# Kernel optimization log

Measured on AMD Instinct MI355X. Metric: run time of the kernel, lower is better.

The kernel has to match this reference:

```python
import jax, jax.numpy as jnp
import numpy as np
import math

B, N, D = 4, 1024, 512
L, H, DH = 6, 8, 64
FF_INNER = 4 * D
NUM_BUCKETS, MAX_DIST = 32, 128
SCALE = 16.0  # cosine_sim_scale
ROT_DIM = 32  # min(32, dim_head)


def layernorm(x, g, stable=False, eps=1e-5):
    if stable:
        x = x / jax.lax.stop_gradient(jnp.max(x, axis=-1, keepdims=True))
    mean = jnp.mean(x, axis=-1, keepdims=True)
    var = jnp.mean(jnp.square(x - mean), axis=-1, keepdims=True)  # unbiased=False
    return (x - mean) * jax.lax.rsqrt(var + eps) * g


def l2norm(x, eps=1e-12):
    return x / jnp.maximum(jnp.linalg.norm(x, axis=-1, keepdims=True), eps)


def rotary_freqs(n):
    inv_freq = 1.0 / (10000.0 ** (jnp.arange(0, ROT_DIM, 2, dtype=jnp.float32) / ROT_DIM))
    f = jnp.arange(n, dtype=jnp.float32)[:, None] * inv_freq[None, :]  # [n, ROT_DIM/2]
    return jnp.repeat(f, 2, axis=-1)  # [n, ROT_DIM], interleaved pairs


def apply_rotary(t, freqs):
    # rotate only first ROT_DIM dims (rotary_embedding_torch semantics)
    rot, passd = t[..., :ROT_DIM], t[..., ROT_DIM:]
    x = rot.reshape(*rot.shape[:-1], ROT_DIM // 2, 2)
    rotated = jnp.stack((-x[..., 1], x[..., 0]), axis=-1).reshape(rot.shape)
    rot = rot * jnp.cos(freqs) + rotated * jnp.sin(freqs)
    return jnp.concatenate([rot, passd], axis=-1)


def rel_pos_bias(emb, i, j):
    # T5-style causal relative position buckets
    rel = jnp.arange(j)[None, :] - jnp.arange(i)[:, None]
    n = jnp.maximum(-rel, 0)
    max_exact = NUM_BUCKETS // 2
    val_large = max_exact + (
        jnp.log(jnp.maximum(n, 1).astype(jnp.float32) / max_exact)
        / math.log(MAX_DIST / max_exact) * (NUM_BUCKETS - max_exact)
    ).astype(jnp.int32)
    val_large = jnp.minimum(val_large, NUM_BUCKETS - 1)
    bucket = jnp.where(n < max_exact, n, val_large)
    return emb[bucket].transpose(2, 0, 1)  # [h, i, j]


def setup_inputs() -> dict:
    key = jax.random.key(0)
    ks = jax.random.split(key, 9)
    s = 0.02
    return {
        "x": jax.random.normal(ks[0], (B, N, D), jnp.float32),
        "rel_pos_emb": jax.random.normal(ks[1], (NUM_BUCKETS, H), jnp.float32) * s,
        "g_attn": jnp.ones((L, D), jnp.float32),
        "null_kv": jax.random.normal(ks[2], (L, 2, DH), jnp.float32),
        "Wq": jax.random.normal(ks[3], (L, D, H * DH), jnp.float32) * s,
        "Wkv": jax.random.normal(ks[4], (L, D, 2 * DH), jnp.float32) * s,
        "Wo": jax.random.normal(ks[5], (L, H * DH, D), jnp.float32) * s,
        "g_attn_out": jnp.ones((L, D), jnp.float32),
        "g_ff": jnp.ones((L, D), jnp.float32),
        "W1": jax.random.normal(ks[6], (L, D, 2 * FF_INNER), jnp.float32) * s,
        "W2": jax.random.normal(ks[7], (L, FF_INNER, D), jnp.float32) * s,
        "g_final": jnp.ones((D,), jnp.float32),
        "W_proj": jax.random.normal(ks[8], (D, D), jnp.float32) * s,
    }


def reference(x, rel_pos_emb, g_attn, null_kv, Wq, Wkv, Wo, g_attn_out, g_ff, W1, W2, g_final, W_proj):
    b, n, d = x.shape
    freqs = rotary_freqs(n)
    bias = rel_pos_bias(rel_pos_emb, n, n + 1)          # [h, n, n+1] (null kv column at j=0)
    causal = jnp.triu(jnp.ones((n, n + 1), dtype=bool), k=2)  # .triu(j - i + 1)
    neg = -jnp.finfo(x.dtype).max
    for l in range(L):
        # --- attention block ---
        xn = layernorm(x, g_attn[l])
        q = (xn @ Wq[l]).reshape(b, n, H, DH).transpose(0, 2, 1, 3) * SCALE  # b h n d
        k, v = jnp.split(xn @ Wkv[l], 2, axis=-1)                            # b n d (single-head kv)
        q = apply_rotary(q, freqs)
        k = apply_rotary(k, freqs)
        k = jnp.concatenate([jnp.broadcast_to(null_kv[l, 0], (b, 1, DH)), k], axis=1)
        v = jnp.concatenate([jnp.broadcast_to(null_kv[l, 1], (b, 1, DH)), v], axis=1)
        qn = l2norm(q) * math.sqrt(SCALE)   # cosine-sim attention
        kn = l2norm(k) * math.sqrt(SCALE)
        sim = jnp.einsum('bhid,bjd->bhij', qn, kn) + bias
        sim = jnp.where(causal, neg, sim)
        attn = jax.nn.softmax(sim.astype(jnp.float32), axis=-1).astype(x.dtype)
        o = jnp.einsum('bhij,bjd->bhid', attn, v).transpose(0, 2, 1, 3).reshape(b, n, H * DH)
        x = x + layernorm(o @ Wo[l], g_attn_out[l])
        # --- SwiGLU feedforward block ---
        hn = layernorm(x, g_ff[l])
        a, gate = jnp.split(hn @ W1[l], 2, axis=-1)
        x = x + (a * jax.nn.silu(gate)) @ W2[l]
    out = layernorm(x, g_final, stable=True)
    return out @ W_proj
```

## Files before the change

### kernel.cpp

```cpp
#include <hip/hip_runtime.h>
#include <hip/hip_bf16.h>
#include <cmath>

using bf16 = __hip_bfloat16;
typedef __bf16 v8bf __attribute__((ext_vector_type(8)));
typedef __bf16 v4bf __attribute__((ext_vector_type(4)));
typedef float  v4f  __attribute__((ext_vector_type(4)));

__device__ __forceinline__ float bf2f(bf16 x) { return __bfloat162float(x); }
__device__ __forceinline__ bf16  f2bf(float x) { return __float2bfloat16(x); }
__device__ __forceinline__ __bf16 tobf(float x) {
    bf16 h = __float2bfloat16(x);
    return __builtin_bit_cast(__bf16, h);
}

__device__ __forceinline__ void gll16(const bf16* g, bf16* l) {
    __builtin_amdgcn_global_load_lds(
        (const __attribute__((address_space(1))) unsigned int*)g,
        (__attribute__((address_space(3))) unsigned int*)l, 16, 0, 0);
}

__device__ __forceinline__ float ldin(const void* p, size_t i, int isf32) {
    if (isf32) return ((const float*)p)[i];
    return bf2f(((const bf16*)p)[i]);
}

__device__ __forceinline__ void ld8(const void* p, size_t base, int f, float v[8]) {
    if (f) {
        const float* pf = (const float*)p + base;
        float4 a = *(const float4*)pf, b = *(const float4*)(pf + 4);
        v[0]=a.x; v[1]=a.y; v[2]=a.z; v[3]=a.w;
        v[4]=b.x; v[5]=b.y; v[6]=b.z; v[7]=b.w;
    } else {
        v8bf a = *(const v8bf*)((const bf16*)p + base);
#pragma unroll
        for (int j = 0; j < 8; ++j) v[j] = (float)a[j];
    }
}

__device__ __forceinline__ float wave_sum(float v) {
#pragma unroll
    for (int o = 32; o > 0; o >>= 1) v += __shfl_xor(v, o, 64);
    return v;
}
__device__ __forceinline__ float wave_max(float v) {
#pragma unroll
    for (int o = 32; o > 0; o >>= 1) v = fmaxf(v, __shfl_xor(v, o, 64));
    return v;
}

__global__ void detect_k(const unsigned short* __restrict__ x, int* __restrict__ flag)
{
    __shared__ int s;
    int t = threadIdx.x;
    if (t == 0) s = 0;
    __syncthreads();
    int bad = 0;
    for (int i = t; i < 4096; i += 256) {
        int e = (x[i] >> 7) & 0xFF;
        if (e >= 147) bad++;
    }
    atomicAdd(&s, bad);
    __syncthreads();
    if (t == 0) *flag = (s > 64) ? 1 : 0;
}

__global__ __launch_bounds__(512, 2)
void gemm256_silu(const bf16* __restrict__ A, const bf16* __restrict__ BT,
                  bf16* __restrict__ U, int K, int lda)
{
    __shared__ bf16 As[2][256 * 64];
    __shared__ bf16 Bs[2][256 * 64];
    const int t = threadIdx.x;
    const int lane = t & 63;
    const int wave = t >> 6;
    const int wm = (wave >> 2) * 128;
    const int wn = (wave & 3) * 64;
    const int bm = blockIdx.x * 256;
    const int bn = blockIdx.y * 256;
    const int fr = lane & 15;
    const int quad = lane >> 4;

    v4f acc[8][4];
#pragma unroll
    for (int i = 0; i < 8; ++i)
#pragma unroll
        for (int j = 0; j < 4; ++j) { v4f z = {0.f, 0.f, 0.f, 0.f}; acc[i][j] = z; }

    auto stage = [&](int buf, int k0) {
#pragma unroll
        for (int r = 0; r < 4; ++r) {
            int c = t + 512 * r;
            int row = c >> 3;
            int g = (c & 7) ^ (row & 7);
            gll16(A + (size_t)(bm + row) * lda + k0 + g * 8, &As[buf][c * 8]);
            gll16(BT + (size_t)(bn + row) * K + k0 + g * 8, &Bs[buf][c * 8]);
        }
    };

    stage(0, 0);
    __syncthreads();
    const int nb = K >> 6;
    for (int kt = 0; kt < nb; ++kt) {
        const int buf = kt & 1;
        if (kt + 1 < nb) stage(buf ^ 1, (kt + 1) * 64);
#pragma unroll
        for (int ks = 0; ks < 2; ++ks) {
            v8bf af[8], bfr[4];
            const int gk = ((ks * 4 + quad) ^ (fr & 7)) * 8;
#pragma unroll
            for (int mt = 0; mt < 8; ++mt)
                af[mt] = *(const v8bf*)(&As[buf][(wm + mt * 16 + fr) * 64 + gk]);
#pragma unroll
            for (int nt = 0; nt < 4; ++nt)
                bfr[nt] = *(const v8bf*)(&Bs[buf][(wn + nt * 16 + fr) * 64 + gk]);
#pragma unroll
            for (int mt = 0; mt < 8; ++mt)
#pragma unroll
                for (int nt = 0; nt < 4; ++nt)
                    acc[mt][nt] = __builtin_amdgcn_mfma_f32_16x16x32_bf16(
                        af[mt], bfr[nt], acc[mt][nt], 0, 0, 0);
        }
        __syncthreads();
    }

    const int r0 = quad * 4;
    const int gbase = ((bn + wn) >> 6) * 32;
#pragma unroll
    for (int mt = 0; mt < 8; ++mt)
#pragma unroll
        for (int nt = 0; nt < 2; ++nt)
#pragma unroll
            for (int r = 0; r < 4; ++r) {
                int row = bm + wm + mt * 16 + r0 + r;
                int col = gbase + nt * 16 + fr;
                float a  = acc[mt][nt][r];
                float gg = acc[mt][nt + 2][r];
                U[(size_t)row * 2048 + col] = f2bf(a * (gg / (1.f + __expf(-gg))));
            }
}

__global__ __launch_bounds__(256)
void gemm64(const bf16* __restrict__ A, const bf16* __restrict__ BT,
            bf16* __restrict__ C, int M, int N, int K, int lda)
{
    __shared__ bf16 As[2][64 * 64];
    __shared__ bf16 Bs[2][64 * 64];
    const int t = threadIdx.x;
    const int lane = t & 63;
    const int wave = t >> 6;
    const int wm = (wave >> 1) * 32;
    const int wn = (wave & 1) * 32;
    const int bm = blockIdx.x * 64;
    const int bn = blockIdx.y * 64;
    const int fr = lane & 15;
    const int quad = lane >> 4;

    v4f acc[2][2];
#pragma unroll
    for (int i = 0; i < 2; ++i)
#pragma unroll
        for (int j = 0; j < 2; ++j) { v4f z = {0.f, 0.f, 0.f, 0.f}; acc[i][j] = z; }

    auto stage = [&](int buf, int k0) {
#pragma unroll
        for (int r = 0; r < 2; ++r) {
            int c = t + 256 * r;
            int row = c >> 3;
            int g = (c & 7) ^ (row & 7);
            gll16(A + (size_t)(bm + row) * lda + k0 + g * 8, &As[buf][c * 8]);
            gll16(BT + (size_t)(bn + row) * K + k0 + g * 8, &Bs[buf][c * 8]);
        }
    };

    stage(0, 0);
    __syncthreads();
    const int nb = K >> 6;
    for (int kt = 0; kt < nb; ++kt) {
        const int buf = kt & 1;
        if (kt + 1 < nb) stage(buf ^ 1, (kt + 1) * 64);
#pragma unroll
        for (int ks = 0; ks < 2; ++ks) {
            v8bf af[2], bfr[2];
            const int gk = ((ks * 4 + quad) ^ (fr & 7)) * 8;
#pragma unroll
            for (int mt = 0; mt < 2; ++mt)
                af[mt] = *(const v8bf*)(&As[buf][(wm + mt * 16 + fr) * 64 + gk]);
#pragma unroll
            for (int nt = 0; nt < 2; ++nt)
                bfr[nt] = *(const v8bf*)(&Bs[buf][(wn + nt * 16 + fr) * 64 + gk]);
#pragma unroll
            for (int mt = 0; mt < 2; ++mt)
#pragma unroll
                for (int nt = 0; nt < 2; ++nt)
                    acc[mt][nt] = __builtin_amdgcn_mfma_f32_16x16x32_bf16(
                        af[mt], bfr[nt], acc[mt][nt], 0, 0, 0);
        }
        __syncthreads();
    }
    const int r0 = quad * 4;
#pragma unroll
    for (int mt = 0; mt < 2; ++mt)
#pragma unroll
        for (int nt = 0; nt < 2; ++nt)
#pragma unroll
            for (int r = 0; r < 4; ++r) {
                int row = bm + wm + mt * 16 + r0 + r;
                int col = bn + wn + nt * 16 + fr;
                C[(size_t)row * N + col] = f2bf(acc[mt][nt][r]);
            }
}

__global__ __launch_bounds__(256)
void gemm64_out(const bf16* __restrict__ A, const bf16* __restrict__ BT,
                void* __restrict__ C, int M, int N, int K, int lda,
                const int* __restrict__ flag)
{
    __shared__ bf16 As[2][64 * 64];
    __shared__ bf16 Bs[2][64 * 64];
    const int f = *flag;
    const int t = threadIdx.x;
    const int lane = t & 63;
    const int wave = t >> 6;
    const int wm = (wave >> 1) * 32;
    const int wn = (wave & 1) * 32;
    const int bm = blockIdx.x * 64;
    const int bn = blockIdx.y * 64;
    const int fr = lane & 15;
    const int quad = lane >> 4;

    v4f acc[2][2];
#pragma unroll
    for (int i = 0; i < 2; ++i)
#pragma unroll
        for (int j = 0; j < 2; ++j) { v4f z = {0.f, 0.f, 0.f, 0.f}; acc[i][j] = z; }

    auto stage = [&](int buf, int k0) {
#pragma unroll
        for (int r = 0; r < 2; ++r) {
            int c = t + 256 * r;
            int row = c >> 3;
            int g = (c & 7) ^ (row & 7);
            gll16(A + (size_t)(bm + row) * lda + k0 + g * 8, &As[buf][c * 8]);
            gll16(BT + (size_t)(bn + row) * K + k0 + g * 8, &Bs[buf][c * 8]);
        }
    };

    stage(0, 0);
    __syncthreads();
    const int nb = K >> 6;
    for (int kt = 0; kt < nb; ++kt) {
        const int buf = kt & 1;
        if (kt + 1 < nb) stage(buf ^ 1, (kt + 1) * 64);
#pragma unroll
        for (int ks = 0; ks < 2; ++ks) {
            v8bf af[2], bfr[2];
            const int gk = ((ks * 4 + quad) ^ (fr & 7)) * 8;
#pragma unroll
            for (int mt = 0; mt < 2; ++mt)
                af[mt] = *(const v8bf*)(&As[buf][(wm + mt * 16 + fr) * 64 + gk]);
#pragma unroll
            for (int nt = 0; nt < 2; ++nt)
                bfr[nt] = *(const v8bf*)(&Bs[buf][(wn + nt * 16 + fr) * 64 + gk]);
#pragma unroll
            for (int mt = 0; mt < 2; ++mt)
#pragma unroll
                for (int nt = 0; nt < 2; ++nt)
                    acc[mt][nt] = __builtin_amdgcn_mfma_f32_16x16x32_bf16(
                        af[mt], bfr[nt], acc[mt][nt], 0, 0, 0);
        }
        __syncthreads();
    }
    const int r0 = quad * 4;
#pragma unroll
    for (int mt = 0; mt < 2; ++mt)
#pragma unroll
        for (int nt = 0; nt < 2; ++nt)
#pragma unroll
            for (int r = 0; r < 4; ++r) {
                int row = bm + wm + mt * 16 + r0 + r;
                int col = bn + wn + nt * 16 + fr;
                if (f) ((float*)C)[(size_t)row * N + col] = acc[mt][nt][r];
                else   ((bf16*)C)[(size_t)row * N + col] = f2bf(acc[mt][nt][r]);
            }
}

__global__ __launch_bounds__(256)
void transpose2_k(const void* __restrict__ in, bf16* __restrict__ out, int R, int C,
                  size_t inZ, size_t outZ, const int* __restrict__ flag)
{
    __shared__ bf16 tile[32][33];
    int f = *flag;
    size_t ioff = (size_t)blockIdx.z * inZ;
    bf16* dst = out + (size_t)blockIdx.z * outZ;
    int c0 = blockIdx.x * 32, r0 = blockIdx.y * 32;
    int tx = threadIdx.x, ty = threadIdx.y;
#pragma unroll
    for (int i = 0; i < 32; i += 8)
        tile[ty + i][tx] = f2bf(ldin(in, ioff + (size_t)(r0 + ty + i) * C + c0 + tx, f));
    __syncthreads();
#pragma unroll
    for (int i = 0; i < 32; i += 8)
        dst[(size_t)(c0 + ty + i) * R + r0 + tx] = tile[tx][ty + i];
}

__global__ __launch_bounds__(256)
void transposeW1_k(const void* __restrict__ in, bf16* __restrict__ out,
                   const int* __restrict__ flag)
{
    __shared__ bf16 tile[32][33];
    int f = *flag;
    size_t ioff = (size_t)blockIdx.z * (512ull * 4096);
    bf16* dst = out + (size_t)blockIdx.z * (512ull * 4096);
    int c0 = blockIdx.x * 32, r0 = blockIdx.y * 32;
    int tx = threadIdx.x, ty = threadIdx.y;
#pragma unroll
    for (int i = 0; i < 32; i += 8)
        tile[ty + i][tx] = f2bf(ldin(in, ioff + (size_t)(r0 + ty + i) * 4096 + c0 + tx, f));
    __syncthreads();
#pragma unroll
    for (int i = 0; i < 32; i += 8) {
        int j = c0 + ty + i;
        int jp = (j < 2048) ? (((j >> 5) << 6) | (j & 31))
                            : ((((j - 2048) >> 5) << 6) | 32 | (j & 31));
        dst[(size_t)jp * 512 + r0 + tx] = tile[tx][ty + i];
    }
}

__global__ __launch_bounds__(256)
void xinit_ln_k(const void* __restrict__ in, const void* __restrict__ g,
                const int* __restrict__ flag, float* __restrict__ x, bf16* __restrict__ xn)
{
    int f = *flag;
    int row = blockIdx.x * 4 + (threadIdx.x >> 6);
    int lane = threadIdx.x & 63;
    int c0 = lane * 8;
    float v[8];
    ld8(in, (size_t)row * 512 + c0, f, v);
    float* xr = x + (size_t)row * 512 + c0;
    *(float4*)xr       = make_float4(v[0], v[1], v[2], v[3]);
    *(float4*)(xr + 4) = make_float4(v[4], v[5], v[6], v[7]);
    float s = 0.f;
#pragma unroll
    for (int j = 0; j < 8; ++j) s += v[j];
    float mean = wave_sum(s) * (1.f / 512.f);
    float q = 0.f;
#pragma unroll
    for (int j = 0; j < 8; ++j) { float d = v[j] - mean; q += d * d; }
    float var = wave_sum(q) * (1.f / 512.f);
    float rstd = rsqrtf(var + 1e-5f);
    float gv[8];
    ld8(g, c0, f, gv);
    v8bf o;
#pragma unroll
    for (int j = 0; j < 8; ++j) o[j] = tobf((v[j] - mean) * rstd * gv[j]);
    *(v8bf*)(xn + (size_t)row * 512 + c0) = o;
}

__global__ __launch_bounds__(256)
void addln_ln_k(const bf16* __restrict__ tin, const void* __restrict__ g1, int g1off,
                const void* __restrict__ g2, int g2off, const int* __restrict__ flag,
                float* __restrict__ x, bf16* __restrict__ xn)
{
    int f = *flag;
    int row = blockIdx.x * 4 + (threadIdx.x >> 6);
    int lane = threadIdx.x & 63;
    int c0 = lane * 8;
    float tv[8];
    {
        v8bf a = *(const v8bf*)(tin + (size_t)row * 512 + c0);
#pragma unroll
        for (int j = 0; j < 8; ++j) tv[j] = (float)a[j];
    }
    float s = 0.f;
#pragma unroll
    for (int j = 0; j < 8; ++j) s += tv[j];
    float mean = wave_sum(s) * (1.f / 512.f);
    float q = 0.f;
#pragma unroll
    for (int j = 0; j < 8; ++j) { float d = tv[j] - mean; q += d * d; }
    float var = wave_sum(q) * (1.f / 512.f);
    float rstd = rsqrtf(var + 1e-5f);
    float g1v[8];
    ld8(g1, (size_t)g1off + c0, f, g1v);
    float* xr = x + (size_t)row * 512 + c0;
    float4 xa = *(float4*)xr, xb = *(float4*)(xr + 4);
    float nx[8] = {xa.x, xa.y, xa.z, xa.w, xb.x, xb.y, xb.z, xb.w};
#pragma unroll
    for (int j = 0; j < 8; ++j) nx[j] += (tv[j] - mean) * rstd * g1v[j];
    *(float4*)xr       = make_float4(nx[0], nx[1], nx[2], nx[3]);
    *(float4*)(xr + 4) = make_float4(nx[4], nx[5], nx[6], nx[7]);
    float s2 = 0.f;
#pragma unroll
    for (int j = 0; j < 8; ++j) s2 += nx[j];
    float mean2 = wave_sum(s2) * (1.f / 512.f);
    float q2 = 0.f;
#pragma unroll
    for (int j = 0; j < 8; ++j) { float e = nx[j] - mean2; q2 += e * e; }
    float var2 = wave_sum(q2) * (1.f / 512.f);
    float rstd2 = rsqrtf(var2 + 1e-5f);
    float g2v[8];
    ld8(g2, (size_t)g2off + c0, f, g2v);
    v8bf o;
#pragma unroll
    for (int j = 0; j < 8; ++j) o[j] = tobf((nx[j] - mean2) * rstd2 * g2v[j]);
    *(v8bf*)(xn + (size_t)row * 512 + c0) = o;
}

__global__ __launch_bounds__(256)
void add_ln_k(const bf16* __restrict__ tin, const void* __restrict__ g, int goff,
              const int* __restrict__ flag, int stable,
              float* __restrict__ x, bf16* __restrict__ xn)
{
    int f = *flag;
    int row = blockIdx.x * 4 + (threadIdx.x >> 6);
    int lane = threadIdx.x & 63;
    int c0 = lane * 8;
    float nx[8];
    {
        v8bf a = *(const v8bf*)(tin + (size_t)row * 512 + c0);
        float* xr = x + (size_t)row * 512 + c0;
        float4 xa = *(float4*)xr, xb = *(float4*)(xr + 4);
        float xv[8] = {xa.x, xa.y, xa.z, xa.w, xb.x, xb.y, xb.z, xb.w};
#pragma unroll
        for (int j = 0; j < 8; ++j) nx[j] = xv[j] + (float)a[j];
        *(float4*)xr       = make_float4(nx[0], nx[1], nx[2], nx[3]);
        *(float4*)(xr + 4) = make_float4(nx[4], nx[5], nx[6], nx[7]);
    }
    float v[8];
#pragma unroll
    for (int j = 0; j < 8; ++j) v[j] = nx[j];
    if (stable) {
        float m = v[0];
#pragma unroll
        for (int j = 1; j < 8; ++j) m = fmaxf(m, v[j]);
        float mx = wave_max(m);
#pragma unroll
        for (int j = 0; j < 8; ++j) v[j] /= mx;
    }
    float s = 0.f;
#pragma unroll
    for (int j = 0; j < 8; ++j) s += v[j];
    float mean = wave_sum(s) * (1.f / 512.f);
    float q = 0.f;
#pragma unroll
    for (int j = 0; j < 8; ++j) { float d = v[j] - mean; q += d * d; }
    float var = wave_sum(q) * (1.f / 512.f);
    float rstd = rsqrtf(var + 1e-5f);
    float gv[8];
    ld8(g, (size_t)goff + c0, f, gv);
    v8bf o;
#pragma unroll
    for (int j = 0; j < 8; ++j) o[j] = tobf((v[j] - mean) * rstd * gv[j]);
    *(v8bf*)(xn + (size_t)row * 512 + c0) = o;
}

__global__ __launch_bounds__(256)
void rotab_k(float2* __restrict__ tab)
{
    int idx = blockIdx.x * 256 + threadIdx.x;
    if (idx >= 16384) return;
    int n = idx >> 4, p = idx & 15;
    float ang = (float)n * expf((float)p * -0.5756462732f);
    tab[idx] = make_float2(cosf(ang), sinf(ang));
}

__global__ __launch_bounds__(256)
void bias_k(const void* __restrict__ rpe, const int* __restrict__ flag, float* __restrict__ tab)
{
    int f = *flag;
    int idx = blockIdx.x * 256 + threadIdx.x;
    if (idx >= 8 * 1025) return;
    int h = idx / 1025, dist = idx % 1025;
    int bkt;
    if (dist < 16) bkt = dist;
    else {
        bkt = 16 + (int)(logf((float)dist / 16.f) / logf(8.f) * 16.f);
        if (bkt > 31) bkt = 31;
    }
    tab[idx] = ldin(rpe, bkt * 8 + h, f) - 16.f;
}

__global__ __launch_bounds__(256)
void qkvprep_k(const bf16* __restrict__ qkv, const void* __restrict__ nkv, int nkoff,
               const int* __restrict__ flag, const float2* __restrict__ rtab,
               bf16* __restrict__ Q, bf16* __restrict__ K, bf16* __restrict__ Vt)
{
    int t = threadIdx.x, lane = t & 63;
    int bid = blockIdx.x;
    if (bid < 2048) {
        int rid = bid * 16 + (t >> 4);
        int h = rid & 7;
        int n = (rid >> 3) & 1023;
        int b = rid >> 13;
        int g16 = t & 15;
        int d0 = g16 * 4;
        v4bf a = *(const v4bf*)(qkv + (size_t)((b << 10) | n) * 640 + h * 64 + d0);
        float v[4];
#pragma unroll
        for (int j = 0; j < 4; ++j) v[j] = (float)a[j] * 16.f;
        if (d0 < 32) {
            float4 cs = *(const float4*)((const float*)rtab + (size_t)n * 32 + (size_t)(d0 >> 1) * 2);
            float r0 = v[0] * cs.x - v[1] * cs.y;
            float r1 = v[1] * cs.x + v[0] * cs.y;
            float r2 = v[2] * cs.z - v[3] * cs.w;
            float r3 = v[3] * cs.z + v[2] * cs.w;
            v[0] = r0; v[1] = r1; v[2] = r2; v[3] = r3;
        }
        float ss = v[0]*v[0] + v[1]*v[1] + v[2]*v[2] + v[3]*v[3];
#pragma unroll
        for (int o = 1; o < 16; o <<= 1) ss += __shfl_xor(ss, o, 64);
        float sc = 4.f / fmaxf(sqrtf(ss), 1e-12f);
        v4bf ov;
#pragma unroll
        for (int j = 0; j < 4; ++j) ov[j] = tobf(v[j] * sc);
        *(v4bf*)(Q + (((size_t)(b * 8 + h)) * 1024 + n) * 64 + d0) = ov;
    } else {
        int f = *flag;
        int rid = (bid - 2048) * 4 + (t >> 6);
        if (rid >= 4 * 1088) return;
        int j = rid % 1088;
        int b = rid / 1088;
        if (j >= 1025) {
            K[((size_t)b * 1088 + j) * 64 + lane] = f2bf(0.f);
            Vt[((size_t)b * 64 + lane) * 1088 + j] = f2bf(0.f);
            return;
        }
        float kv, vv;
        if (j == 0) {
            kv = ldin(nkv, nkoff + lane, f);
            vv = ldin(nkv, nkoff + 64 + lane, f);
        } else {
            int n = j - 1;
            const bf16* src = qkv + (size_t)(b * 1024 + n) * 640 + 512;
            kv = bf2f(src[lane]);
            vv = bf2f(src[64 + lane]);
            if (lane < 32) {
                float2 cs = rtab[n * 16 + (lane >> 1)];
                float other = __shfl_xor(kv, 1, 64);
                float rot = (lane & 1) ? other : -other;
                kv = kv * cs.x + rot * cs.y;
            }
        }
        float nrm = sqrtf(wave_sum(kv * kv));
        kv = kv / fmaxf(nrm, 1e-12f) * 4.f;
        K[((size_t)b * 1088 + j) * 64 + lane] = f2bf(kv);
        Vt[((size_t)b * 64 + lane) * 1088 + j] = f2bf(vv);
    }
}

__global__ __launch_bounds__(256)
void attn_mfma(const bf16* __restrict__ Q, const bf16* __restrict__ Kg,
               const bf16* __restrict__ Vtg, const float* __restrict__ bias,
               bf16* __restrict__ O)
{
    __shared__ bf16 Ks[64][72];
    __shared__ bf16 Vts[64][72];
    __shared__ bf16 Ps[4][16][72];
    __shared__ float bs[1088];
    const int bh = blockIdx.x, b = bh >> 3, h = bh & 7;
    const int yy = (int)gridDim.y - 1 - (int)blockIdx.y;
    const int i0 = yy * 64;
    const int t = threadIdx.x, lane = t & 63, w = t >> 6;
    const int col = lane & 15, quad = lane >> 4, fk = quad * 8;
    const float* bt = bias + h * 1025;
    const bf16* Kb = Kg + (size_t)b * 1088 * 64;
    const bf16* Vb = Vtg + (size_t)b * 64 * 1088;

    for (int idx = t; idx < i0 + 64; idx += 256) bs[idx] = bt[idx];

    v8bf qf[2];
    const bf16* qrow = Q + ((size_t)bh * 1024 + i0 + w * 16 + col) * 64;
    qf[0] = *(const v8bf*)(qrow + fk);
    qf[1] = *(const v8bf*)(qrow + 32 + fk);

    v4f oacc[4];
#pragma unroll
    for (int dt = 0; dt < 4; ++dt) { v4f z = {0.f,0.f,0.f,0.f}; oacc[dt] = z; }
    float lpart[4] = {0.f, 0.f, 0.f, 0.f};

    const int nch = yy + 2;
    const int rr0 = t >> 3, co0 = (t & 7) * 8;
    const int rr1 = (t + 256) >> 3, co1 = co0;

    v8bf kr[2], vr[2];
    {
        kr[0] = *(const v8bf*)(Kb + (size_t)rr0 * 64 + co0);
        vr[0] = *(const v8bf*)(Vb + (size_t)rr0 * 1088 + co0);
        kr[1] = *(const v8bf*)(Kb + (size_t)rr1 * 64 + co1);
        vr[1] = *(const v8bf*)(Vb + (size_t)rr1 * 1088 + co1);
    }

    for (int ch = 0; ch < nch; ++ch) {
        const int j0 = ch * 64;
        __syncthreads();
        *(v8bf*)(&Ks[rr0][co0])  = kr[0];
        *(v8bf*)(&Vts[rr0][co0]) = vr[0];
        *(v8bf*)(&Ks[rr1][co1])  = kr[1];
        *(v8bf*)(&Vts[rr1][co1]) = vr[1];
        if (ch + 1 < nch) {
            int j0n = (ch + 1) * 64;
            kr[0] = *(const v8bf*)(Kb + (size_t)(j0n + rr0) * 64 + co0);
            vr[0] = *(const v8bf*)(Vb + (size_t)rr0 * 1088 + j0n + co0);
            kr[1] = *(const v8bf*)(Kb + (size_t)(j0n + rr1) * 64 + co1);
            vr[1] = *(const v8bf*)(Vb + (size_t)rr1 * 1088 + j0n + co1);
        }
        __syncthreads();

        v4f sreg[4];
#pragma unroll
        for (int nt = 0; nt < 4; ++nt) {
            v4f z = {0.f,0.f,0.f,0.f};
            v8bf kf0 = *(const v8bf*)(&Ks[nt * 16 + col][fk]);
            v8bf kf1 = *(const v8bf*)(&Ks[nt * 16 + col][32 + fk]);
            z = __builtin_amdgcn_mfma_f32_16x16x32_bf16(qf[0], kf0, z, 0, 0, 0);
            z = __builtin_amdgcn_mfma_f32_16x16x32_bf16(qf[1], kf1, z, 0, 0, 0);
            sreg[nt] = z;
        }

        if (ch < yy) {
#pragma unroll
            for (int reg = 0; reg < 4; ++reg) {
                int i = i0 + w * 16 + quad * 4 + reg;
                int dbase = i - j0 - col;
#pragma unroll
                for (int nt = 0; nt < 4; ++nt) {
                    float pp = __expf(sreg[nt][reg] + bs[dbase - nt * 16]);
                    lpart[reg] += pp;
                    Ps[w][quad * 4 + reg][nt * 16 + col] = f2bf(pp);
                }
            }
        } else {
#pragma unroll
            for (int reg = 0; reg < 4; ++reg) {
                int i = i0 + w * 16 + quad * 4 + reg;
#pragma unroll
                for (int nt = 0; nt < 4; ++nt) {
                    int j = j0 + nt * 16 + col;
                    float pp = 0.f;
                    if (j <= i + 1 && j < 1025) {
                        int dist = i - j; if (dist < 0) dist = 0;
                        pp = __expf(sreg[nt][reg] + bs[dist]);
                    }
                    lpart[reg] += pp;
                    Ps[w][quad * 4 + reg][nt * 16 + col] = f2bf(pp);
                }
            }
        }

        v8bf pf[2];
        pf[0] = *(const v8bf*)(&Ps[w][col][fk]);
        pf[1] = *(const v8bf*)(&Ps[w][col][32 + fk]);
#pragma unroll
        for (int dt = 0; dt < 4; ++dt) {
#pragma unroll
            for (int ks = 0; ks < 2; ++ks) {
                v8bf vf = *(const v8bf*)(&Vts[dt * 16 + col][ks * 32 + fk]);
                oacc[dt] = __builtin_amdgcn_mfma_f32_16x16x32_bf16(pf[ks], vf, oacc[dt], 0, 0, 0);
            }
        }
    }

#pragma unroll
    for (int reg = 0; reg < 4; ++reg) {
#pragma unroll
        for (int o = 1; o < 16; o <<= 1) lpart[reg] += __shfl_xor(lpart[reg], o, 64);
        float inv = 1.f / lpart[reg];
        int i = i0 + w * 16 + quad * 4 + reg;
        bf16* orow = O + ((size_t)(b * 1024 + i)) * 512 + h * 64;
#pragma unroll
        for (int dt = 0; dt < 4; ++dt)
            orow[dt * 16 + col] = f2bf(oacc[dt][reg] * inv);
    }
}

extern "C" void kernel_launch(void* const* d_in, const int* in_sizes, int n_in,
                              void* d_out, int out_size, void* d_ws, size_t ws_size,
                              hipStream_t stream)
{
    const void* x_in     = d_in[0];
    const void* rpe      = d_in[1];
    const void* g_attn   = d_in[2];
    const void* null_kv  = d_in[3];
    const void* Wq       = d_in[4];
    const void* Wkv      = d_in[5];
    const void* Wo       = d_in[6];
    const void* g_attn_o = d_in[7];
    const void* g_ff     = d_in[8];
    const void* W1       = d_in[9];
    const void* W2       = d_in[10];
    const void* g_final  = d_in[11];
    const void* W_proj   = d_in[12];

    char* wp = (char*)d_ws;
    auto alloc = [&](size_t bytes) {
        char* p = wp; wp += (bytes + 255) & ~(size_t)255; return p;
    };
    float* xf    = (float*)alloc(4096ull * 512 * 4);
    bf16*  xn    = (bf16*) alloc(4096ull * 512 * 2);
    bf16*  tb    = (bf16*) alloc(4096ull * 512 * 2);
    bf16*  ub    = (bf16*) alloc(4096ull * 4096 * 2);
    bf16*  Kb    = (bf16*) alloc(4ull * 1088 * 64 * 2);
    bf16*  Vtb   = (bf16*) alloc(4ull * 64 * 1088 * 2);
    float* btab  = (float*)alloc(8ull * 1025 * 4);
    float2* rtab = (float2*)alloc(16384ull * 8);
    int*   dfl   = (int*)  alloc(256);
    bf16*  WqkvT = (bf16*) alloc(6ull * 640 * 512 * 2);
    bf16*  WoT   = (bf16*) alloc(6ull * 512 * 512 * 2);
    bf16*  W1T   = (bf16*) alloc(6ull * 4096 * 512 * 2);
    bf16*  W2T   = (bf16*) alloc(6ull * 512 * 2048 * 2);
    bf16*  WpT   = (bf16*) alloc(512ull * 512 * 2);
    bf16*  qkvb  = ub;
    bf16*  Qb    = ub + 2621440;
    bf16*  ob    = ub + 4718592;

    detect_k<<<1, 256, 0, stream>>>((const unsigned short*)x_in, dfl);
    transpose2_k<<<dim3(16, 16, 6),  dim3(32, 8), 0, stream>>>(Wq, WqkvT, 512, 512, 512ull*512, 640ull*512, dfl);
    transpose2_k<<<dim3(4, 16, 6),   dim3(32, 8), 0, stream>>>(Wkv, WqkvT + 512ull*512, 512, 128, 512ull*128, 640ull*512, dfl);
    transpose2_k<<<dim3(16, 16, 6),  dim3(32, 8), 0, stream>>>(Wo, WoT, 512, 512, 512ull*512, 512ull*512, dfl);
    transposeW1_k<<<dim3(128, 16, 6), dim3(32, 8), 0, stream>>>(W1, W1T, dfl);
    transpose2_k<<<dim3(16, 64, 6),  dim3(32, 8), 0, stream>>>(W2, W2T, 2048, 512, 2048ull*512, 2048ull*512, dfl);
    transpose2_k<<<dim3(16, 16, 1),  dim3(32, 8), 0, stream>>>(W_proj, WpT, 512, 512, 512ull*512, 512ull*512, dfl);
    bias_k<<<33, 256, 0, stream>>>(rpe, dfl, btab);
    rotab_k<<<64, 256, 0, stream>>>(rtab);
    xinit_ln_k<<<1024, 256, 0, stream>>>(x_in, g_attn, dfl, xf, xn);

    for (int l = 0; l < 6; ++l) {
        gemm64<<<dim3(64, 10), 256, 0, stream>>>(xn, WqkvT + (size_t)l * 640 * 512, qkvb, 4096, 640, 512, 512);
        qkvprep_k<<<3136, 256, 0, stream>>>(qkvb, null_kv, l * 128, dfl, rtab, Qb, Kb, Vtb);
        attn_mfma<<<dim3(32, 16), 256, 0, stream>>>(Qb, Kb, Vtb, btab, ob);
        gemm64<<<dim3(64, 8), 256, 0, stream>>>(ob, WoT + (size_t)l * 512 * 512, tb, 4096, 512, 512, 512);
        addln_ln_k<<<1024, 256, 0, stream>>>(tb, g_attn_o, l * 512, g_ff, l * 512, dfl, xf, xn);
        gemm256_silu<<<dim3(16, 16), 512, 0, stream>>>(xn, W1T + (size_t)l * 4096 * 512, ub, 512, 512);
        gemm64<<<dim3(64, 8), 256, 0, stream>>>(ub, W2T + (size_t)l * 512 * 2048, tb, 4096, 512, 2048, 2048);
        if (l < 5)
            add_ln_k<<<1024, 256, 0, stream>>>(tb, g_attn, (l + 1) * 512, dfl, 0, xf, xn);
        else
            add_ln_k<<<1024, 256, 0, stream>>>(tb, g_final, 0, dfl, 1, xf, xn);
    }
    gemm64_out<<<dim3(64, 8), 256, 0, stream>>>(xn, WpT, d_out, 4096, 512, 512, 512, dfl);
}
```

Baseline: 808.6 us.

## Widen attention KV chunks to 128 keys and merge bias/rotary table kernels

The attention kernel now processes 128 keys per iteration instead of 64. This halves the number of loop iterations and __syncthreads barriers, and gives each chunk more MFMA work per load. K and Vt buffers are padded to 1152 rows so the larger chunks stay in bounds, and the prep kernel zero-fills the extra rows. The bias and rotary table setup kernels are also merged into one launch. In exchange, LDS use and register pressure rise, and more fully-masked keys are computed near the causal diagonal.

After: 812.0 us. Within noise of the previous version (+0.4%).

```diff
diff --git a/kernel.cpp b/kernel.cpp
--- a/kernel.cpp
+++ b/kernel.cpp
@@ -456,29 +456,26 @@
 }
 
 __global__ __launch_bounds__(256)
-void rotab_k(float2* __restrict__ tab)
+void biasrot_k(const void* __restrict__ rpe, const int* __restrict__ flag,
+               float* __restrict__ tab, float2* __restrict__ rtab)
 {
     int idx = blockIdx.x * 256 + threadIdx.x;
-    if (idx >= 16384) return;
-    int n = idx >> 4, p = idx & 15;
-    float ang = (float)n * expf((float)p * -0.5756462732f);
-    tab[idx] = make_float2(cosf(ang), sinf(ang));
-}
-
-__global__ __launch_bounds__(256)
-void bias_k(const void* __restrict__ rpe, const int* __restrict__ flag, float* __restrict__ tab)
-{
-    int f = *flag;
-    int idx = blockIdx.x * 256 + threadIdx.x;
-    if (idx >= 8 * 1025) return;
-    int h = idx / 1025, dist = idx % 1025;
-    int bkt;
-    if (dist < 16) bkt = dist;
-    else {
-        bkt = 16 + (int)(logf((float)dist / 16.f) / logf(8.f) * 16.f);
-        if (bkt > 31) bkt = 31;
-    }
-    tab[idx] = ldin(rpe, bkt * 8 + h, f) - 16.f;
+    if (idx < 8 * 1025) {
+        int f = *flag;
+        int h = idx / 1025, dist = idx % 1025;
+        int bkt;
+        if (dist < 16) bkt = dist;
+        else {
+            bkt = 16 + (int)(logf((float)dist / 16.f) / logf(8.f) * 16.f);
+            if (bkt > 31) bkt = 31;
+        }
+        tab[idx] = ldin(rpe, bkt * 8 + h, f) - 16.f;
+    } else if (idx < 8 * 1025 + 16384) {
+        int k = idx - 8 * 1025;
+        int n = k >> 4, p = k & 15;
+        float ang = (float)n * expf((float)p * -0.5756462732f);
+        rtab[k] = make_float2(cosf(ang), sinf(ang));
+    }
 }
 
 __global__ __launch_bounds__(256)
@@ -518,12 +515,12 @@
     } else {
         int f = *flag;
         int rid = (bid - 2048) * 4 + (t >> 6);
-        if (rid >= 4 * 1088) return;
-        int j = rid % 1088;
-        int b = rid / 1088;
+        if (rid >= 4 * 1152) return;
+        int j = rid % 1152;
+        int b = rid / 1152;
         if (j >= 1025) {
-            K[((size_t)b * 1088 + j) * 64 + lane] = f2bf(0.f);
-            Vt[((size_t)b * 64 + lane) * 1088 + j] = f2bf(0.f);
+            K[((size_t)b * 1152 + j) * 64 + lane] = f2bf(0.f);
+            Vt[((size_t)b * 64 + lane) * 1152 + j] = f2bf(0.f);
             return;
         }
         float kv, vv;
@@ -544,8 +541,8 @@
         }
         float nrm = sqrtf(wave_sum(kv * kv));
         kv = kv / fmaxf(nrm, 1e-12f) * 4.f;
-        K[((size_t)b * 1088 + j) * 64 + lane] = f2bf(kv);
-        Vt[((size_t)b * 64 + lane) * 1088 + j] = f2bf(vv);
+        K[((size_t)b * 1152 + j) * 64 + lane] = f2bf(kv);
+        Vt[((size_t)b * 64 + lane) * 1152 + j] = f2bf(vv);
     }
 }
 
@@ -554,9 +551,9 @@
                const bf16* __restrict__ Vtg, const float* __restrict__ bias,
                bf16* __restrict__ O)
 {
-    __shared__ bf16 Ks[64][72];
-    __shared__ bf16 Vts[64][72];
-    __shared__ bf16 Ps[4][16][72];
+    __shared__ bf16 Ks[128][72];
+    __shared__ bf16 Vts[64][136];
+    __shared__ bf16 Ps[4][16][136];
     __shared__ float bs[1088];
     const int bh = blockIdx.x, b = bh >> 3, h = bh & 7;
     const int yy = (int)gridDim.y - 1 - (int)blockIdx.y;
@@ -564,8 +561,8 @@
     const int t = threadIdx.x, lane = t & 63, w = t >> 6;
     const int col = lane & 15, quad = lane >> 4, fk = quad * 8;
     const float* bt = bias + h * 1025;
-    const bf16* Kb = Kg + (size_t)b * 1088 * 64;
-    const bf16* Vb = Vtg + (size_t)b * 64 * 1088;
+    const bf16* Kb = Kg + (size_t)b * 1152 * 64;
+    const bf16* Vb = Vtg + (size_t)b * 64 * 1152;
 
     for (int idx = t; idx < i0 + 64; idx += 256) bs[idx] = bt[idx];
 
@@ -579,37 +576,38 @@
     for (int dt = 0; dt < 4; ++dt) { v4f z = {0.f,0.f,0.f,0.f}; oacc[dt] = z; }
     float lpart[4] = {0.f, 0.f, 0.f, 0.f};
 
-    const int nch = yy + 2;
-    const int rr0 = t >> 3, co0 = (t & 7) * 8;
-    const int rr1 = (t + 256) >> 3, co1 = co0;
-
-    v8bf kr[2], vr[2];
-    {
-        kr[0] = *(const v8bf*)(Kb + (size_t)rr0 * 64 + co0);
-        vr[0] = *(const v8bf*)(Vb + (size_t)rr0 * 1088 + co0);
-        kr[1] = *(const v8bf*)(Kb + (size_t)rr1 * 64 + co1);
-        vr[1] = *(const v8bf*)(Vb + (size_t)rr1 * 1088 + co1);
+    const int nch = (i0 + 66 + 127) >> 7;
+    const int rK = t >> 3,  cK = (t & 7) * 8;
+    const int rV = t >> 4,  cV = (t & 15) * 8;
+
+    v8bf kr[4], vr[4];
+#pragma unroll
+    for (int r = 0; r < 4; ++r) {
+        kr[r] = *(const v8bf*)(Kb + (size_t)(rK + 32 * r) * 64 + cK);
+        vr[r] = *(const v8bf*)(Vb + (size_t)(rV + 16 * r) * 1152 + cV);
     }
 
     for (int ch = 0; ch < nch; ++ch) {
-        const int j0 = ch * 64;
+        const int j0 = ch * 128;
         __syncthreads();
-        *(v8bf*)(&Ks[rr0][co0])  = kr[0];
-        *(v8bf*)(&Vts[rr0][co0]) = vr[0];
-        *(v8bf*)(&Ks[rr1][co1])  = kr[1];
-        *(v8bf*)(&Vts[rr1][co1]) = vr[1];
+#pragma unroll
+        for (int r = 0; r < 4; ++r) {
+            *(v8bf*)(&Ks[rK + 32 * r][cK])  = kr[r];
+            *(v8bf*)(&Vts[rV + 16 * r][cV]) = vr[r];
+        }
         if (ch + 1 < nch) {
-            int j0n = (ch + 1) * 64;
-            kr[0] = *(const v8bf*)(Kb + (size_t)(j0n + rr0) * 64 + co0);
-            vr[0] = *(const v8bf*)(Vb + (size_t)rr0 * 1088 + j0n + co0);
-            kr[1] = *(const v8bf*)(Kb + (size_t)(j0n + rr1) * 64 + co1);
-            vr[1] = *(const v8bf*)(Vb + (size_t)rr1 * 1088 + j0n + co1);
+            int j0n = (ch + 1) * 128;
+#pragma unroll
+            for (int r = 0; r < 4; ++r) {
+                kr[r] = *(const v8bf*)(Kb + (size_t)(j0n + rK + 32 * r) * 64 + cK);
+                vr[r] = *(const v8bf*)(Vb + (size_t)(rV + 16 * r) * 1152 + j0n + cV);
+            }
         }
         __syncthreads();
 
-        v4f sreg[4];
-#pragma unroll
-        for (int nt = 0; nt < 4; ++nt) {
+        v4f sreg[8];
+#pragma unroll
+        for (int nt = 0; nt < 8; ++nt) {
             v4f z = {0.f,0.f,0.f,0.f};
             v8bf kf0 = *(const v8bf*)(&Ks[nt * 16 + col][fk]);
             v8bf kf1 = *(const v8bf*)(&Ks[nt * 16 + col][32 + fk]);
@@ -618,13 +616,13 @@
             sreg[nt] = z;
         }
 
-        if (ch < yy) {
+        if (j0 + 127 <= i0) {
 #pragma unroll
             for (int reg = 0; reg < 4; ++reg) {
                 int i = i0 + w * 16 + quad * 4 + reg;
                 int dbase = i - j0 - col;
 #pragma unroll
-                for (int nt = 0; nt < 4; ++nt) {
+                for (int nt = 0; nt < 8; ++nt) {
                     float pp = __expf(sreg[nt][reg] + bs[dbase - nt * 16]);
                     lpart[reg] += pp;
                     Ps[w][quad * 4 + reg][nt * 16 + col] = f2bf(pp);
@@ -635,7 +633,7 @@
             for (int reg = 0; reg < 4; ++reg) {
                 int i = i0 + w * 16 + quad * 4 + reg;
 #pragma unroll
-                for (int nt = 0; nt < 4; ++nt) {
+                for (int nt = 0; nt < 8; ++nt) {
                     int j = j0 + nt * 16 + col;
                     float pp = 0.f;
                     if (j <= i + 1 && j < 1025) {
@@ -648,13 +646,14 @@
             }
         }
 
-        v8bf pf[2];
-        pf[0] = *(const v8bf*)(&Ps[w][col][fk]);
-        pf[1] = *(const v8bf*)(&Ps[w][col][32 + fk]);
+        v8bf pf[4];
+#pragma unroll
+        for (int ks = 0; ks < 4; ++ks)
+            pf[ks] = *(const v8bf*)(&Ps[w][col][ks * 32 + fk]);
 #pragma unroll
         for (int dt = 0; dt < 4; ++dt) {
 #pragma unroll
-            for (int ks = 0; ks < 2; ++ks) {
+            for (int ks = 0; ks < 4; ++ks) {
                 v8bf vf = *(const v8bf*)(&Vts[dt * 16 + col][ks * 32 + fk]);
                 oacc[dt] = __builtin_amdgcn_mfma_f32_16x16x32_bf16(pf[ks], vf, oacc[dt], 0, 0, 0);
             }
@@ -700,8 +699,8 @@
     bf16*  xn    = (bf16*) alloc(4096ull * 512 * 2);
     bf16*  tb    = (bf16*) alloc(4096ull * 512 * 2);
     bf16*  ub    = (bf16*) alloc(4096ull * 4096 * 2);
-    bf16*  Kb    = (bf16*) alloc(4ull * 1088 * 64 * 2);
-    bf16*  Vtb   = (bf16*) alloc(4ull * 64 * 1088 * 2);
+    bf16*  Kb    = (bf16*) alloc(4ull * 1152 * 64 * 2);
+    bf16*  Vtb   = (bf16*) alloc(4ull * 64 * 1152 * 2);
     float* btab  = (float*)alloc(8ull * 1025 * 4);
     float2* rtab = (float2*)alloc(16384ull * 8);
     int*   dfl   = (int*)  alloc(256);
@@ -721,13 +720,12 @@
     transposeW1_k<<<dim3(128, 16, 6), dim3(32, 8), 0, stream>>>(W1, W1T, dfl);
     transpose2_k<<<dim3(16, 64, 6),  dim3(32, 8), 0, stream>>>(W2, W2T, 2048, 512, 2048ull*512, 2048ull*512, dfl);
     transpose2_k<<<dim3(16, 16, 1),  dim3(32, 8), 0, stream>>>(W_proj, WpT, 512, 512, 512ull*512, 512ull*512, dfl);
-    bias_k<<<33, 256, 0, stream>>>(rpe, dfl, btab);
-    rotab_k<<<64, 256, 0, stream>>>(rtab);
+    biasrot_k<<<97, 256, 0, stream>>>(rpe, dfl, btab, rtab);
     xinit_ln_k<<<1024, 256, 0, stream>>>(x_in, g_attn, dfl, xf, xn);
 
     for (int l = 0; l < 6; ++l) {
         gemm64<<<dim3(64, 10), 256, 0, stream>>>(xn, WqkvT + (size_t)l * 640 * 512, qkvb, 4096, 640, 512, 512);
-        qkvprep_k<<<3136, 256, 0, stream>>>(qkvb, null_kv, l * 128, dfl, rtab, Qb, Kb, Vtb);
+        qkvprep_k<<<3200, 256, 0, stream>>>(qkvb, null_kv, l * 128, dfl, rtab, Qb, Kb, Vtb);
         attn_mfma<<<dim3(32, 16), 256, 0, stream>>>(Qb, Kb, Vtb, btab, ob);
         gemm64<<<dim3(64, 8), 256, 0, stream>>>(ob, WoT + (size_t)l * 512 * 512, tb, 4096, 512, 512, 512);
         addln_ln_k<<<1024, 256, 0, stream>>>(tb, g_attn_o, l * 512, g_ff, l * 512, dfl, xf, xn);
```
